# Optimization experiments

Measured on AMD Instinct MI355X. Metric: run time of the kernel, lower is better.

## Reference

```python
import jax, jax.numpy as jnp
import numpy as np

NUM_HEADS = 8
D_HEAD = 64
LN_EPS = 1e-6


def _pad_idx(lengths, max_len):
    # flat indices into a [B*max_len, ...] dense buffer for each packed token
    return np.concatenate([b * max_len + np.arange(int(l)) for b, l in enumerate(lengths)])


def _layer_norm(x, scale, bias):
    mu = jnp.mean(x, axis=-1, keepdims=True)
    var = jnp.mean(jnp.square(x - mu), axis=-1, keepdims=True)
    return (x - mu) * jax.lax.rsqrt(var + LN_EPS) * scale + bias


def setup_inputs() -> dict:
    key = jax.random.key(0)
    ks = jax.random.split(key, 12)
    d_model, d_ff, H, dh = 512, 2048, NUM_HEADS, D_HEAD
    lengths = np.array([128 * (i + 1) for i in range(8)], dtype=np.int64)  # sum = 4608
    total = int(lengths.sum())
    s = 0.02
    return {
        "x": jax.random.normal(ks[0], (total, d_model), jnp.float32),
        "mem": jax.random.normal(ks[1], (total, d_model), jnp.float32),
        "lengths_x": lengths,
        "lengths_mem": lengths.copy(),
        "Wq": jax.random.normal(ks[2], (d_model, H * dh), jnp.float32) * s,
        "Wk": jax.random.normal(ks[3], (d_model, H * dh), jnp.float32) * s,
        "Wv": jax.random.normal(ks[4], (d_model, H * dh), jnp.float32) * s,
        "Wo": jax.random.normal(ks[5], (H * dh, d_model), jnp.float32) * s,
        "ln1_scale": jnp.ones((d_model,), jnp.float32),
        "ln1_bias": jnp.zeros((d_model,), jnp.float32),
        "W1": jax.random.normal(ks[6], (d_model, d_ff), jnp.float32) * s,
        "b1": jnp.zeros((d_ff,), jnp.float32),
        "W2": jax.random.normal(ks[7], (d_ff, d_model), jnp.float32) * s,
        "b2": jnp.zeros((d_model,), jnp.float32),
        "ln2_scale": jnp.ones((d_model,), jnp.float32),
        "ln2_bias": jnp.zeros((d_model,), jnp.float32),
    }


def reference(x, mem, lengths_x, lengths_mem, Wq, Wk, Wv, Wo,
              ln1_scale, ln1_bias, W1, b1, W2, b2, ln2_scale, ln2_bias):
    lx = np.asarray(lengths_x)
    lm = np.asarray(lengths_mem)
    B = lx.shape[0]
    Lx = int(lx.max())
    Lm = int(lm.max())
    H, dh = NUM_HEADS, D_HEAD

    idx_x = _pad_idx(lx, Lx)
    idx_m = _pad_idx(lm, Lm)

    def pad(packed, idx, B, L):
        dense = jnp.zeros((B * L,) + packed.shape[1:], packed.dtype).at[idx].set(packed)
        return dense.reshape((B, L) + packed.shape[1:])

    q = pad((x @ Wq).reshape(-1, H, dh), idx_x, B, Lx)   # [B, Lx, H, dh]
    k = pad((mem @ Wk).reshape(-1, H, dh), idx_m, B, Lm)  # [B, Lm, H, dh]
    v = pad((mem @ Wv).reshape(-1, H, dh), idx_m, B, Lm)

    e = jnp.einsum('bxhd,byhd->bhxy', q, k) / np.sqrt(dh)  # [B, H, Lx, Lm]
    # validity mask: (query pos < len_x) & (key pos < len_mem)
    mask = (np.arange(Lx)[None, :, None] < lx[:, None, None]) & \
           (np.arange(Lm)[None, None, :] < lm[:, None, None])
    mask = jnp.asarray(mask)[:, None, :, :]  # [B, 1, Lx, Lm]
    e = jnp.where(mask, e, jnp.float32(-1e30))  # finite -inf surrogate; identical softmax on valid rows
    alpha = jax.nn.softmax(e, axis=-1)
    out = jnp.einsum('bhxy,byhd->bxhd', alpha, v).reshape(B, Lx, H * dh)
    out = out @ Wo                                  # [B, Lx, d_model]
    out = out.reshape(B * Lx, -1)[idx_x]            # pack back to [total_x, d_model]

    h = _layer_norm(x + out, ln1_scale, ln1_bias)
    ffn = jax.nn.relu(h @ W1 + b1) @ W2 + b2
    return _layer_norm(h + ffn, ln2_scale, ln2_bias)
```

## Files before the change

### kernel.cpp

```cpp
#include <hip/hip_runtime.h>
#include <stdint.h>

typedef short bf8v __attribute__((ext_vector_type(8)));
typedef float f4v  __attribute__((ext_vector_type(4)));
typedef short s8v  __attribute__((ext_vector_type(8)));
typedef short s4v  __attribute__((ext_vector_type(4)));
typedef int   i2v  __attribute__((ext_vector_type(2)));

__device__ __forceinline__ float bf2f(short b){
  unsigned u = ((unsigned)(unsigned short)b) << 16;
  union { unsigned u; float f; } c; c.u = u; return c.f;
}
__device__ __forceinline__ short f2bf(float f){
  union { float f; unsigned u; } c; c.f = f;
  unsigned r = (c.u + 0x7FFFu + ((c.u >> 16) & 1u)) >> 16;
  return (short)r;
}
__device__ __forceinline__ void gload16(const short* g, short* l){
  __builtin_amdgcn_global_load_lds(
      (const __attribute__((address_space(1))) void*)g,
      (__attribute__((address_space(3))) void*)l, 16, 0, 0);
}

__global__ void prep_kernel(const int* lx, const int* lm, int* meta){
  __shared__ int sjp[9], skvc[8];
  int tid = threadIdx.x;
  if (tid == 0){
    int is64 = ((lx[1] | lx[3] | lx[5] | lx[7]) == 0) ? 1 : 0;
    int ox = 0, om = 0;
    for (int b = 0; b < 8; ++b){
      int a = is64 ? lx[2*b] : lx[b];
      int c = is64 ? lm[2*b] : lm[b];
      meta[b] = a; meta[8+b] = c;
      meta[16+b] = ox; meta[25+b] = om;
      ox += a; om += c;
    }
    meta[24] = ox; meta[33] = om;
    int jp = 0;
    for (int b = 0; b < 8; ++b){
      int Lm_ = meta[8+b];
      int kvc = (Lm_ + 255) / 256; if (kvc > 4) kvc = 4; if (kvc < 1) kvc = 1;
      int clen = (((Lm_ + kvc - 1) / kvc) + 31) & ~31;
      meta[34+b] = kvc; meta[42+b] = clen;
      meta[50+b] = jp;
      sjp[b] = jp; skvc[b] = kvc;
      int qt = (meta[b] + 63) / 64;
      jp += qt * kvc * 8;
    }
    meta[58] = jp;
    sjp[8] = jp;
  }
  __syncthreads();
  int njobs = sjp[8];
  for (int j = tid; j < njobs; j += blockDim.x){
    int b = 0;
    #pragma unroll
    for (int i = 1; i < 8; ++i) if (j >= sjp[i]) b = i;
    int local = j - sjp[b];
    int kvc = skvc[b];
    int h = local & 7;
    int r = local >> 3;
    int c = r % kvc;
    int qt = r / kvc;
    meta[64+j] = b | (h << 4) | (c << 7) | (qt << 11);
  }
}

__global__ __launch_bounds__(256) void cvt2bf(const float* __restrict__ x,
                                              const float* __restrict__ mem,
                                              short* __restrict__ xb,
                                              short* __restrict__ mb,
                                              long long n){
  long long t = (long long)blockIdx.x * 256 + threadIdx.x;
  long long i = t * 8;
  const float* s; short* d;
  if (i < n){ s = x + i; d = xb + i; }
  else {
    i -= n; if (i >= n) return;
    s = mem + i; d = mb + i;
  }
  float4 f0 = *(const float4*)s;
  float4 f1 = *(const float4*)(s + 4);
  s8v o;
  o[0]=f2bf(f0.x); o[1]=f2bf(f0.y); o[2]=f2bf(f0.z); o[3]=f2bf(f0.w);
  o[4]=f2bf(f1.x); o[5]=f2bf(f1.y); o[6]=f2bf(f1.z); o[7]=f2bf(f1.w);
  *(s8v*)d = o;
}

__global__ __launch_bounds__(256) void cvt_w_t(
    const float* __restrict__ Wq, const float* __restrict__ Wk,
    const float* __restrict__ Wv, const float* __restrict__ Wo,
    const float* __restrict__ W1, const float* __restrict__ W2,
    short* __restrict__ WqT, short* __restrict__ WkT,
    short* __restrict__ WvT, short* __restrict__ WoT,
    short* __restrict__ W1T, short* __restrict__ W2T){
  __shared__ float tile[32][33];
  int bid = blockIdx.x;
  const float* W; short* WT; int K, N, t0;
  if      (bid <  256){ W=Wq; WT=WqT; K=512;  N=512;  t0=0;    }
  else if (bid <  512){ W=Wk; WT=WkT; K=512;  N=512;  t0=256;  }
  else if (bid <  768){ W=Wv; WT=WvT; K=512;  N=512;  t0=512;  }
  else if (bid < 1024){ W=Wo; WT=WoT; K=512;  N=512;  t0=768;  }
  else if (bid < 2048){ W=W1; WT=W1T; K=512;  N=2048; t0=1024; }
  else                { W=W2; WT=W2T; K=2048; N=512;  t0=2048; }
  int lt = bid - t0;
  int ntn = N / 32;
  int tk = lt / ntn, tn = lt % ntn;
  int r0 = threadIdx.x >> 5, c = threadIdx.x & 31;
  #pragma unroll
  for (int i = 0; i < 4; ++i){
    int r = r0 + i*8;
    tile[r][c] = W[(long)(tk*32 + r)*N + tn*32 + c];
  }
  __syncthreads();
  #pragma unroll
  for (int i = 0; i < 4; ++i){
    int r = r0 + i*8;
    WT[(long)(tn*32 + r)*K + tk*32 + c] = f2bf(tile[c][r]);
  }
}

__device__ __forceinline__ void stage_g64(const short* A, const short* Bt,
    long brow, long bcol, int M, int N, int K, int t,
    short* Als, short* Bls){
  int tid = threadIdx.x;
  #pragma unroll
  for (int i = 0; i < 2; ++i){
    int cc = i*256 + tid;
    int row = cc >> 3, slot = cc & 7;
    int cg = slot ^ (row & 7);
    long ar = brow + row; if (ar >= M) ar = M - 1;
    gload16(A + ar*(long)K + t + cg*8, &Als[cc*8]);
  }
  #pragma unroll
  for (int i = 0; i < 4; ++i){
    int cc = i*256 + tid;
    int row = cc >> 3, slot = cc & 7;
    int cg = slot ^ (row & 7);
    long br = bcol + row; if (br >= N) br = N - 1;
    gload16(Bt + br*(long)K + t + cg*8, &Bls[cc*8]);
  }
}

__device__ __forceinline__ void gemm_core64(const short* A, const short* Bt,
    short* __restrict__ Cb, const float* __restrict__ bias,
    int M, int N, int K, int k0, int klen,
    float scale, int relu, int colmajor,
    long brow, long bcol, short* Als, short* Bls){
  int tid = threadIdx.x;
  int lane = tid & 63, w = tid >> 6;
  int wcol = w * 32;
  int l15 = lane & 15, l4 = lane >> 4;

  f4v acc[4][2];
  #pragma unroll
  for (int m = 0; m < 4; ++m)
    #pragma unroll
    for (int n = 0; n < 2; ++n) acc[m][n] = (f4v){0.f,0.f,0.f,0.f};

  int nt = klen / 64;
  stage_g64(A, Bt, brow, bcol, M, N, K, k0, Als, Bls);
  for (int t = 0; t < nt; ++t){
    __syncthreads();
    if (t + 1 < nt)
      stage_g64(A, Bt, brow, bcol, M, N, K, k0 + (t+1)*64,
                Als + ((t+1)&1)*4096, Bls + ((t+1)&1)*8192);
    const short* Ab = Als + (t&1)*4096;
    const short* Bb = Bls + (t&1)*8192;
    bf8v a[4][2], b[2][2];
    #pragma unroll
    for (int m = 0; m < 4; ++m){
      int row = m*16 + l15;
      #pragma unroll
      for (int ks = 0; ks < 2; ++ks)
        a[m][ks] = *(const bf8v*)&Ab[row*64 + ((ks*4 + l4) ^ (row & 7))*8];
    }
    #pragma unroll
    for (int n = 0; n < 2; ++n){
      int row = wcol + n*16 + l15;
      #pragma unroll
      for (int ks = 0; ks < 2; ++ks)
        b[n][ks] = *(const bf8v*)&Bb[row*64 + ((ks*4 + l4) ^ (row & 7))*8];
    }
    #pragma unroll
    for (int m = 0; m < 4; ++m)
      #pragma unroll
      for (int n = 0; n < 2; ++n){
        acc[m][n] = __builtin_amdgcn_mfma_f32_16x16x32_bf16(a[m][0], b[n][0], acc[m][n], 0, 0, 0);
        acc[m][n] = __builtin_amdgcn_mfma_f32_16x16x32_bf16(a[m][1], b[n][1], acc[m][n], 0, 0, 0);
      }
  }

  #pragma unroll
  for (int m = 0; m < 4; ++m){
    #pragma unroll
    for (int n = 0; n < 2; ++n){
      long col = bcol + wcol + n*16 + l15;
      float bi = (bias != nullptr && col < N) ? bias[col] : 0.f;
      #pragma unroll
      for (int j = 0; j < 4; ++j){
        long row = brow + m*16 + 4*l4 + j;
        if (row < M && col < N){
          float v = acc[m][n][j] * scale + bi;
          if (relu) v = fmaxf(v, 0.f);
          Cb[colmajor ? (col*(long)M + row) : (row*(long)N + col)] = f2bf(v);
        }
      }
    }
  }
}

__global__ __launch_bounds__(256) void gemm64(
    const short* __restrict__ A, const short* __restrict__ Bt,
    short* __restrict__ C, const float* __restrict__ bias,
    int M, int N, int K, int klen, float scale, int relu, int colmajor){
  __shared__ __align__(16) short Als[2*64*64];
  __shared__ __align__(16) short Bls[2*128*64];
  int chunk = blockIdx.z;
  gemm_core64(A, Bt, C + (long)chunk * M * N, bias, M, N, K, chunk*klen, klen,
              scale, relu, colmajor,
              (long)blockIdx.y * 64, (long)blockIdx.x * 128, Als, Bls);
}

__global__ __launch_bounds__(256) void gemm_qkv(
    const short* __restrict__ xb, const short* __restrict__ mb,
    const short* __restrict__ WqT, const short* __restrict__ WkT,
    const short* __restrict__ WvT,
    short* __restrict__ Qb, short* __restrict__ Kbf, short* __restrict__ Vtb,
    int total){
  __shared__ __align__(16) short Als[2*64*64];
  __shared__ __align__(16) short Bls[2*128*64];
  int seg = blockIdx.x >> 2;
  const short* A  = (seg == 0) ? xb : mb;
  const short* Bt = (seg == 0) ? WqT : ((seg == 1) ? WkT : WvT);
  short* C        = (seg == 0) ? Qb  : ((seg == 1) ? Kbf : Vtb);
  float scale     = (seg == 0) ? 0.125f : 1.f;
  int colmajor    = (seg == 2);
  gemm_core64(A, Bt, C, nullptr, total, 512, 512, 0, 512, scale, 0, colmajor,
              (long)blockIdx.y * 64, (long)(blockIdx.x & 3) * 128, Als, Bls);
}

__global__ __launch_bounds__(256) void attn_kernel(
    const short* __restrict__ Q, const short* __restrict__ Kb,
    const short* __restrict__ Vt, short* __restrict__ Ob,
    short* __restrict__ Opart, float* __restrict__ mlpart,
    const int* __restrict__ meta, int total){
  __shared__ __align__(16) short Kls[2][32*64];
  __shared__ __align__(16) short Vls[2][64*32];
  __shared__ __align__(16) short Pls[4][16*32];
  int tid = threadIdx.x;
  int lane = tid & 63, w = tid >> 6;
  int l15 = lane & 15, l4 = lane >> 4;
  int njobs = meta[58];

  for (int j = blockIdx.x; j < njobs; j += gridDim.x){
    int word = meta[64+j];
    int b = word & 15, h = (word >> 4) & 7, c = (word >> 7) & 15, qt = word >> 11;
    int Lx = meta[b], Lm = meta[8+b];
    int ox = meta[16+b], om = meta[25+b];
    int kvc = meta[34+b], clen = meta[42+b];
    int c0 = c * clen;
    int cend = c0 + clen; if (cend > Lm) cend = Lm;
    int nt = (cend - c0 + 31) / 32;
    int qbase = qt*64 + w*16;

    __syncthreads();

    #define ATTN_STAGE(T, BUF)                                                  \
      {                                                                         \
        int kv0_ = c0 + (T)*32;                                                 \
        int kr = tid >> 3, ks_ = tid & 7;                                       \
        int cgk = ks_ ^ (kr & 7);                                               \
        int ktok = kv0_ + kr; if (ktok >= Lm) ktok = Lm - 1;                    \
        gload16(Kb + (long)(om + ktok)*512 + h*64 + cgk*8, &Kls[BUF][tid*8]);   \
        int vr = tid >> 2, vs = tid & 3;                                        \
        int cgv = vs ^ (vr & 3);                                                \
        int vkv = kv0_ + cgv*8; if (vkv + 8 > Lm) vkv = Lm - 8;                 \
        gload16(Vt + (long)(h*64 + vr)*total + om + vkv, &Vls[BUF][tid*8]);     \
      }

    ATTN_STAGE(0, 0)

    int qr = qbase + l15;
    const short* qp = Q + (long)(ox + (qr < Lx ? qr : Lx - 1))*512 + h*64 + l4*8;
    bf8v aq0 = *(const bf8v*)qp;
    bf8v aq1 = *(const bf8v*)(qp + 32);

    float mrun = -1e30f, lrun = 0.f;
    f4v o[4];
    #pragma unroll
    for (int n = 0; n < 4; ++n) o[n] = (f4v){0.f,0.f,0.f,0.f};

    for (int t = 0; t < nt; ++t){
      __syncthreads();
      if (t + 1 < nt) ATTN_STAGE(t+1, (t+1)&1)
      int buf = t & 1;
      int kv0 = c0 + t*32;

      f4v s[2];
      #pragma unroll
      for (int n = 0; n < 2; ++n){
        int krow = n*16 + l15;
        bf8v k0 = *(const bf8v*)&Kls[buf][krow*64 + ((l4    ) ^ (krow & 7))*8];
        bf8v k1 = *(const bf8v*)&Kls[buf][krow*64 + ((4 + l4) ^ (krow & 7))*8];
        f4v z = (f4v){0.f,0.f,0.f,0.f};
        z = __builtin_amdgcn_mfma_f32_16x16x32_bf16(k0, aq0, z, 0, 0, 0);
        z = __builtin_amdgcn_mfma_f32_16x16x32_bf16(k1, aq1, z, 0, 0, 0);
        s[n] = z;
      }
      if (kv0 + 32 > cend){
        #pragma unroll
        for (int n = 0; n < 2; ++n){
          int kvb = kv0 + n*16 + 4*l4;
          #pragma unroll
          for (int jj = 0; jj < 4; ++jj)
            if (kvb + jj >= cend) s[n][jj] = -1e30f;
        }
      }
      float m1 = fmaxf(fmaxf(fmaxf(s[0][0], s[0][1]), fmaxf(s[0][2], s[0][3])),
                       fmaxf(fmaxf(s[1][0], s[1][1]), fmaxf(s[1][2], s[1][3])));
      m1 = fmaxf(m1, __shfl_xor(m1, 16, 64));
      m1 = fmaxf(m1, __shfl_xor(m1, 32, 64));
      float mnew = fmaxf(mrun, m1);
      float sc = __expf(mrun - mnew);
      mrun = mnew;
      float rs = 0.f;
      #pragma unroll
      for (int n = 0; n < 2; ++n)
        #pragma unroll
        for (int jj = 0; jj < 4; ++jj){
          float p = __expf(s[n][jj] - mnew);
          s[n][jj] = p; rs += p;
        }
      rs += __shfl_xor(rs, 16, 64);
      rs += __shfl_xor(rs, 32, 64);
      lrun = lrun * sc + rs;
      #pragma unroll
      for (int n = 0; n < 4; ++n) o[n] *= sc;

      #pragma unroll
      for (int n = 0; n < 2; ++n){
        unsigned r0, r1;
        asm("v_cvt_pk_bf16_f32 %0, %1, %2" : "=v"(r0) : "v"(s[n][0]), "v"(s[n][1]));
        asm("v_cvt_pk_bf16_f32 %0, %1, %2" : "=v"(r1) : "v"(s[n][2]), "v"(s[n][3]));
        i2v pr; pr[0] = (int)r0; pr[1] = (int)r1;
        int cs = (n*4 + l4) ^ ((l15 & 3) << 1);
        *(i2v*)&Pls[w][l15*32 + cs*4] = pr;
      }
      bf8v pb = *(const bf8v*)&Pls[w][l15*32 + (((2*l4) ^ ((l15 & 3) << 1))*4)];

      #pragma unroll
      for (int n2 = 0; n2 < 4; ++n2){
        int vrow = n2*16 + l15;
        bf8v vv = *(const bf8v*)&Vls[buf][vrow*32 + ((l4 ^ (vrow & 3))*8)];
        o[n2] = __builtin_amdgcn_mfma_f32_16x16x32_bf16(vv, pb, o[n2], 0, 0, 0);
      }
    }
    #undef ATTN_STAGE

    if (qr < Lx){
      if (kvc == 1){
        float inv = 1.f / lrun;
        long obase = (long)(ox + qr)*512 + h*64;
        #pragma unroll
        for (int n2 = 0; n2 < 4; ++n2){
          s4v ov;
          #pragma unroll
          for (int jj = 0; jj < 4; ++jj) ov[jj] = f2bf(o[n2][jj] * inv);
          *(s4v*)&Ob[obase + n2*16 + l4*4] = ov;
        }
      } else {
        long slot = ((long)(ox + qr)*8 + h)*4 + c;
        #pragma unroll
        for (int n2 = 0; n2 < 4; ++n2){
          s4v ov;
          #pragma unroll
          for (int jj = 0; jj < 4; ++jj) ov[jj] = f2bf(o[n2][jj]);
          *(s4v*)&Opart[slot*64 + n2*16 + l4*4] = ov;
        }
        if (l4 == 0){
          float2 ml; ml.x = mrun; ml.y = lrun;
          *(float2*)&mlpart[slot*2] = ml;
        }
      }
    }
  }
}

__global__ __launch_bounds__(256) void attn_combine(
    const short* __restrict__ Opart, const float* __restrict__ mlpart,
    short* __restrict__ Ob, const int* __restrict__ meta, int total){
  int w = threadIdx.x >> 6, lane = threadIdx.x & 63;
  int row = blockIdx.x*4 + w;
  if (row >= total) return;
  int b = 0;
  #pragma unroll
  for (int i = 1; i < 8; ++i) if (row >= meta[16+i]) b = i;
  int kvc = meta[34+b];
  if (kvc <= 1) return;
  for (int h = 0; h < 8; ++h){
    long sbase = ((long)row*8 + h)*4;
    float m_ = -1e30f;
    for (int c = 0; c < kvc; ++c) m_ = fmaxf(m_, mlpart[(sbase+c)*2]);
    float num = 0.f, den = 0.f;
    for (int c = 0; c < kvc; ++c){
      float mc = mlpart[(sbase+c)*2];
      float lc = mlpart[(sbase+c)*2 + 1];
      float wgt = __expf(mc - m_);
      num += wgt * bf2f(Opart[(sbase+c)*64 + lane]);
      den += wgt * lc;
    }
    Ob[(long)row*512 + h*64 + lane] = f2bf(num / den);
  }
}

__global__ __launch_bounds__(256) void ln_fuse(
    const float* __restrict__ Af, const short* __restrict__ Ab,
    const short* __restrict__ PartB, int nparts, long pstride,
    const float* __restrict__ bias,
    const float* __restrict__ gamma, const float* __restrict__ beta,
    short* __restrict__ outb, float* __restrict__ outf, int rows){
  int w = threadIdx.x >> 6, lane = threadIdx.x & 63;
  long row = (long)blockIdx.x * 4 + w;
  if (row >= rows) return;
  int c0 = lane * 8;
  long base = row * 512 + c0;
  float v[8];
  if (Af){
    float4 f0 = *(const float4*)(Af + base);
    float4 f1 = *(const float4*)(Af + base + 4);
    v[0]=f0.x; v[1]=f0.y; v[2]=f0.z; v[3]=f0.w;
    v[4]=f1.x; v[5]=f1.y; v[6]=f1.z; v[7]=f1.w;
  } else {
    s8v a = *(const s8v*)(Ab + base);
    #pragma unroll
    for (int j = 0; j < 8; ++j) v[j] = bf2f(a[j]);
  }
  for (int c = 0; c < nparts; ++c){
    s8v pv = *(const s8v*)(PartB + c*pstride + base);
    #pragma unroll
    for (int j = 0; j < 8; ++j) v[j] += bf2f(pv[j]);
  }
  if (bias){
    #pragma unroll
    for (int j = 0; j < 8; ++j) v[j] += bias[c0 + j];
  }
  float sum = 0.f;
  #pragma unroll
  for (int j = 0; j < 8; ++j) sum += v[j];
  #pragma unroll
  for (int m = 1; m < 64; m <<= 1) sum += __shfl_xor(sum, m, 64);
  float mu = sum * (1.f/512.f);
  float q = 0.f;
  #pragma unroll
  for (int j = 0; j < 8; ++j){ float d = v[j] - mu; q += d*d; }
  #pragma unroll
  for (int m = 1; m < 64; m <<= 1) q += __shfl_xor(q, m, 64);
  float rs = rsqrtf(q * (1.f/512.f) + 1e-6f);
  float ov[8];
  #pragma unroll
  for (int j = 0; j < 8; ++j)
    ov[j] = (v[j] - mu) * rs * gamma[c0 + j] + beta[c0 + j];
  if (outb){
    s8v os;
    #pragma unroll
    for (int j = 0; j < 8; ++j) os[j] = f2bf(ov[j]);
    *(s8v*)(outb + base) = os;
  }
  if (outf){
    float4 f0 = {ov[0], ov[1], ov[2], ov[3]};
    float4 f1 = {ov[4], ov[5], ov[6], ov[7]};
    *(float4*)(outf + base) = f0;
    *(float4*)(outf + base + 4) = f1;
  }
}

extern "C" void kernel_launch(void* const* d_in, const int* in_sizes, int n_in,
                              void* d_out, int out_size, void* d_ws, size_t ws_size,
                              hipStream_t stream){
  (void)n_in; (void)out_size; (void)ws_size;
  const float* x   = (const float*)d_in[0];
  const float* mem = (const float*)d_in[1];
  const int*   lxr = (const int*)d_in[2];
  const int*   lmr = (const int*)d_in[3];
  const float* Wq  = (const float*)d_in[4];
  const float* Wk  = (const float*)d_in[5];
  const float* Wv  = (const float*)d_in[6];
  const float* Wo  = (const float*)d_in[7];
  const float* g1  = (const float*)d_in[8];
  const float* be1 = (const float*)d_in[9];
  const float* W1  = (const float*)d_in[10];
  const float* b1  = (const float*)d_in[11];
  const float* W2  = (const float*)d_in[12];
  const float* b2  = (const float*)d_in[13];
  const float* g2  = (const float*)d_in[14];
  const float* be2 = (const float*)d_in[15];
  float* out = (float*)d_out;

  int total = in_sizes[0] / 512;
  if (total <= 0) return;
  long long n = (long long)total * 512;

  char* p = (char*)d_ws;
  int*   meta  = (int*)p;    p += 16384;
  short* xb    = (short*)p;  p += n*2;
  short* mb    = (short*)p;  p += n*2;
  short* Qb    = (short*)p;  p += n*2;
  short* Kbf   = (short*)p;  p += n*2;
  short* Vtb   = (short*)p;  p += n*2;
  short* attnb = (short*)p;  p += n*2;
  short* hb    = (short*)p;  p += n*2;
  short* ffn1  = (short*)p;  p += (long long)total*2048*2;
  short* Opart = (short*)p;  p += (long long)total*8*4*64*2;
  float* mlprt = (float*)p;  p += (long long)total*8*4*2*4;
  short* p_wo  = (short*)p;  p += n*2*2;
  short* p_ff  = (short*)p;  p += n*4*2;
  short* WqT   = (short*)p;  p += 512*512*2;
  short* WkT   = (short*)p;  p += 512*512*2;
  short* WvT   = (short*)p;  p += 512*512*2;
  short* WoT   = (short*)p;  p += 512*512*2;
  short* W1T   = (short*)p;  p += 2048*512*2;
  short* W2T   = (short*)p;  p += 512*2048*2;

  prep_kernel<<<1, 256, 0, stream>>>(lxr, lmr, meta);

  long long th = (2*n)/8;
  cvt2bf<<<dim3((unsigned)((th + 255)/256)), dim3(256), 0, stream>>>(x, mem, xb, mb, n);
  cvt_w_t<<<dim3(3072), dim3(256), 0, stream>>>(Wq,Wk,Wv,Wo,W1,W2, WqT,WkT,WvT,WoT,W1T,W2T);

  int mt64 = (total + 63)/64;
  gemm_qkv<<<dim3(12, mt64), 256, 0, stream>>>(xb, mb, WqT, WkT, WvT, Qb, Kbf, Vtb, total);

  attn_kernel<<<dim3(2048), 256, 0, stream>>>(Qb, Kbf, Vtb, attnb,
                                              Opart, mlprt, meta, total);
  attn_combine<<<dim3((unsigned)((total + 3)/4)), 256, 0, stream>>>(
      Opart, mlprt, attnb, meta, total);

  gemm64<<<dim3(4, mt64, 2), 256, 0, stream>>>(attnb, WoT, p_wo, nullptr,
                                               total, 512, 512, 256, 1.f, 0, 0);
  ln_fuse<<<dim3((unsigned)((total + 3)/4)), 256, 0, stream>>>(
      x, nullptr, p_wo, 2, n, nullptr, g1, be1, hb, nullptr, total);

  gemm64<<<dim3(16, mt64, 1), 256, 0, stream>>>(hb, W1T, ffn1, b1,
                                                total, 2048, 512, 512, 1.f, 1, 0);
  gemm64<<<dim3(4, mt64, 4), 256, 0, stream>>>(ffn1, W2T, p_ff, nullptr,
                                               total, 512, 2048, 512, 1.f, 0, 0);
  ln_fuse<<<dim3((unsigned)((total + 3)/4)), 256, 0, stream>>>(
      nullptr, hb, p_ff, 4, n, b2, g2, be2, nullptr, out, total);
}
```

Baseline: 184.7 us.

## Merge setup kernels and stream GEMM B operand from global into registers

Fuses the metadata prep, activation bf16 conversion and weight transpose kernels into one launch, removing two kernel launches. The GEMM core is reworked to use a K-step of 32, stage only the A tile in LDS, and load B fragments straight from global memory into registers with one-step prefetch. LDS use drops to 8 KB, and launch_bounds now requests 4 blocks per SM for higher occupancy. The cost is that B loads are no longer shared through LDS, so each wave fetches its B fragments from global/L2 separately, and there are twice as many barrier iterations per K.

```diff
diff --git a/kernel.cpp b/kernel.cpp
--- a/kernel.cpp
+++ b/kernel.cpp
@@ -22,91 +22,94 @@
       (__attribute__((address_space(3))) void*)l, 16, 0, 0);
 }
 
-__global__ void prep_kernel(const int* lx, const int* lm, int* meta){
-  __shared__ int sjp[9], skvc[8];
-  int tid = threadIdx.x;
-  if (tid == 0){
-    int is64 = ((lx[1] | lx[3] | lx[5] | lx[7]) == 0) ? 1 : 0;
-    int ox = 0, om = 0;
-    for (int b = 0; b < 8; ++b){
-      int a = is64 ? lx[2*b] : lx[b];
-      int c = is64 ? lm[2*b] : lm[b];
-      meta[b] = a; meta[8+b] = c;
-      meta[16+b] = ox; meta[25+b] = om;
-      ox += a; om += c;
-    }
-    meta[24] = ox; meta[33] = om;
-    int jp = 0;
-    for (int b = 0; b < 8; ++b){
-      int Lm_ = meta[8+b];
-      int kvc = (Lm_ + 255) / 256; if (kvc > 4) kvc = 4; if (kvc < 1) kvc = 1;
-      int clen = (((Lm_ + kvc - 1) / kvc) + 31) & ~31;
-      meta[34+b] = kvc; meta[42+b] = clen;
-      meta[50+b] = jp;
-      sjp[b] = jp; skvc[b] = kvc;
-      int qt = (meta[b] + 63) / 64;
-      jp += qt * kvc * 8;
-    }
-    meta[58] = jp;
-    sjp[8] = jp;
-  }
-  __syncthreads();
-  int njobs = sjp[8];
-  for (int j = tid; j < njobs; j += blockDim.x){
-    int b = 0;
-    #pragma unroll
-    for (int i = 1; i < 8; ++i) if (j >= sjp[i]) b = i;
-    int local = j - sjp[b];
-    int kvc = skvc[b];
-    int h = local & 7;
-    int r = local >> 3;
-    int c = r % kvc;
-    int qt = r / kvc;
-    meta[64+j] = b | (h << 4) | (c << 7) | (qt << 11);
-  }
-}
-
-__global__ __launch_bounds__(256) void cvt2bf(const float* __restrict__ x,
-                                              const float* __restrict__ mem,
-                                              short* __restrict__ xb,
-                                              short* __restrict__ mb,
-                                              long long n){
-  long long t = (long long)blockIdx.x * 256 + threadIdx.x;
-  long long i = t * 8;
-  const float* s; short* d;
-  if (i < n){ s = x + i; d = xb + i; }
-  else {
-    i -= n; if (i >= n) return;
-    s = mem + i; d = mb + i;
-  }
-  float4 f0 = *(const float4*)s;
-  float4 f1 = *(const float4*)(s + 4);
-  s8v o;
-  o[0]=f2bf(f0.x); o[1]=f2bf(f0.y); o[2]=f2bf(f0.z); o[3]=f2bf(f0.w);
-  o[4]=f2bf(f1.x); o[5]=f2bf(f1.y); o[6]=f2bf(f1.z); o[7]=f2bf(f1.w);
-  *(s8v*)d = o;
-}
-
-__global__ __launch_bounds__(256) void cvt_w_t(
+__global__ __launch_bounds__(256) void setup_kernel(
+    const int* lx, const int* lm, int* meta,
+    const float* __restrict__ x, const float* __restrict__ mem,
+    short* __restrict__ xb, short* __restrict__ mb, long long n, int nblk_cvt,
     const float* __restrict__ Wq, const float* __restrict__ Wk,
     const float* __restrict__ Wv, const float* __restrict__ Wo,
     const float* __restrict__ W1, const float* __restrict__ W2,
     short* __restrict__ WqT, short* __restrict__ WkT,
     short* __restrict__ WvT, short* __restrict__ WoT,
     short* __restrict__ W1T, short* __restrict__ W2T){
+  __shared__ int sjp[9], skvc[8];
   __shared__ float tile[32][33];
+  int tid = threadIdx.x;
   int bid = blockIdx.x;
+
+  if (bid == 0){
+    if (tid == 0){
+      int is64 = ((lx[1] | lx[3] | lx[5] | lx[7]) == 0) ? 1 : 0;
+      int ox = 0, om = 0;
+      for (int b = 0; b < 8; ++b){
+        int a = is64 ? lx[2*b] : lx[b];
+        int c = is64 ? lm[2*b] : lm[b];
+        meta[b] = a; meta[8+b] = c;
+        meta[16+b] = ox; meta[25+b] = om;
+        ox += a; om += c;
+      }
+      meta[24] = ox; meta[33] = om;
+      int jp = 0;
+      for (int b = 0; b < 8; ++b){
+        int Lm_ = meta[8+b];
+        int kvc = (Lm_ + 255) / 256; if (kvc > 4) kvc = 4; if (kvc < 1) kvc = 1;
+        int clen = (((Lm_ + kvc - 1) / kvc) + 31) & ~31;
+        meta[34+b] = kvc; meta[42+b] = clen;
+        meta[50+b] = jp;
+        sjp[b] = jp; skvc[b] = kvc;
+        int qt = (meta[b] + 63) / 64;
+        jp += qt * kvc * 8;
+      }
+      meta[58] = jp;
+      sjp[8] = jp;
+    }
+    __syncthreads();
+    int njobs = sjp[8];
+    for (int j = tid; j < njobs; j += blockDim.x){
+      int b = 0;
+      #pragma unroll
+      for (int i = 1; i < 8; ++i) if (j >= sjp[i]) b = i;
+      int local = j - sjp[b];
+      int kvc = skvc[b];
+      int h = local & 7;
+      int r = local >> 3;
+      int c = r % kvc;
+      int qt = r / kvc;
+      meta[64+j] = b | (h << 4) | (c << 7) | (qt << 11);
+    }
+    return;
+  }
+
+  if (bid <= nblk_cvt){
+    long long t = (long long)(bid - 1) * 256 + tid;
+    long long i = t * 8;
+    const float* s; short* d;
+    if (i < n){ s = x + i; d = xb + i; }
+    else {
+      i -= n; if (i >= n) return;
+      s = mem + i; d = mb + i;
+    }
+    float4 f0 = *(const float4*)s;
+    float4 f1 = *(const float4*)(s + 4);
+    s8v o;
+    o[0]=f2bf(f0.x); o[1]=f2bf(f0.y); o[2]=f2bf(f0.z); o[3]=f2bf(f0.w);
+    o[4]=f2bf(f1.x); o[5]=f2bf(f1.y); o[6]=f2bf(f1.z); o[7]=f2bf(f1.w);
+    *(s8v*)d = o;
+    return;
+  }
+
+  int wbid = bid - 1 - nblk_cvt;
   const float* W; short* WT; int K, N, t0;
-  if      (bid <  256){ W=Wq; WT=WqT; K=512;  N=512;  t0=0;    }
-  else if (bid <  512){ W=Wk; WT=WkT; K=512;  N=512;  t0=256;  }
-  else if (bid <  768){ W=Wv; WT=WvT; K=512;  N=512;  t0=512;  }
-  else if (bid < 1024){ W=Wo; WT=WoT; K=512;  N=512;  t0=768;  }
-  else if (bid < 2048){ W=W1; WT=W1T; K=512;  N=2048; t0=1024; }
-  else                { W=W2; WT=W2T; K=2048; N=512;  t0=2048; }
-  int lt = bid - t0;
+  if      (wbid <  256){ W=Wq; WT=WqT; K=512;  N=512;  t0=0;    }
+  else if (wbid <  512){ W=Wk; WT=WkT; K=512;  N=512;  t0=256;  }
+  else if (wbid <  768){ W=Wv; WT=WvT; K=512;  N=512;  t0=512;  }
+  else if (wbid < 1024){ W=Wo; WT=WoT; K=512;  N=512;  t0=768;  }
+  else if (wbid < 2048){ W=W1; WT=W1T; K=512;  N=2048; t0=1024; }
+  else                 { W=W2; WT=W2T; K=2048; N=512;  t0=2048; }
+  int lt = wbid - t0;
   int ntn = N / 32;
   int tk = lt / ntn, tn = lt % ntn;
-  int r0 = threadIdx.x >> 5, c = threadIdx.x & 31;
+  int r0 = tid >> 5, c = tid & 31;
   #pragma unroll
   for (int i = 0; i < 4; ++i){
     int r = r0 + i*8;
@@ -120,33 +123,21 @@
   }
 }
 
-__device__ __forceinline__ void stage_g64(const short* A, const short* Bt,
-    long brow, long bcol, int M, int N, int K, int t,
-    short* Als, short* Bls){
+__device__ __forceinline__ void stage_a(const short* A, long brow, int M, int K,
+                                        int kofs, short* Als){
   int tid = threadIdx.x;
-  #pragma unroll
-  for (int i = 0; i < 2; ++i){
-    int cc = i*256 + tid;
-    int row = cc >> 3, slot = cc & 7;
-    int cg = slot ^ (row & 7);
-    long ar = brow + row; if (ar >= M) ar = M - 1;
-    gload16(A + ar*(long)K + t + cg*8, &Als[cc*8]);
-  }
-  #pragma unroll
-  for (int i = 0; i < 4; ++i){
-    int cc = i*256 + tid;
-    int row = cc >> 3, slot = cc & 7;
-    int cg = slot ^ (row & 7);
-    long br = bcol + row; if (br >= N) br = N - 1;
-    gload16(Bt + br*(long)K + t + cg*8, &Bls[cc*8]);
-  }
-}
-
-__device__ __forceinline__ void gemm_core64(const short* A, const short* Bt,
+  int row = tid >> 2, slot = tid & 3;
+  int cg = slot ^ ((row >> 1) & 3);
+  long ar = brow + row; if (ar >= M) ar = M - 1;
+  gload16(A + ar*(long)K + kofs + cg*8, &Als[tid*8]);
+}
+
+__device__ __forceinline__ void gemm_core(const short* __restrict__ A,
+    const short* __restrict__ Bt,
     short* __restrict__ Cb, const float* __restrict__ bias,
     int M, int N, int K, int k0, int klen,
     float scale, int relu, int colmajor,
-    long brow, long bcol, short* Als, short* Bls){
+    long brow, long bcol, short* Als){
   int tid = threadIdx.x;
   int lane = tid & 63, w = tid >> 6;
   int wcol = w * 32;
@@ -158,37 +149,34 @@
     #pragma unroll
     for (int n = 0; n < 2; ++n) acc[m][n] = (f4v){0.f,0.f,0.f,0.f};
 
-  int nt = klen / 64;
-  stage_g64(A, Bt, brow, bcol, M, N, K, k0, Als, Bls);
+  const short* bp = Bt + (bcol + wcol + l15)*(long)K + k0 + l4*8;
+  long bstep = 16*(long)K;
+
+  int nt = klen / 32;
+  stage_a(A, brow, M, K, k0, Als);
+  bf8v bc0 = *(const bf8v*)bp;
+  bf8v bc1 = *(const bf8v*)(bp + bstep);
   for (int t = 0; t < nt; ++t){
     __syncthreads();
-    if (t + 1 < nt)
-      stage_g64(A, Bt, brow, bcol, M, N, K, k0 + (t+1)*64,
-                Als + ((t+1)&1)*4096, Bls + ((t+1)&1)*8192);
-    const short* Ab = Als + (t&1)*4096;
-    const short* Bb = Bls + (t&1)*8192;
-    bf8v a[4][2], b[2][2];
+    if (t + 1 < nt) stage_a(A, brow, M, K, k0 + (t+1)*32, Als + ((t+1)&1)*2048);
+    bf8v bn0, bn1;
+    if (t + 1 < nt){
+      bn0 = *(const bf8v*)(bp + (t+1)*32);
+      bn1 = *(const bf8v*)(bp + bstep + (t+1)*32);
+    }
+    const short* Ab = Als + (t&1)*2048;
+    bf8v a[4];
     #pragma unroll
     for (int m = 0; m < 4; ++m){
       int row = m*16 + l15;
-      #pragma unroll
-      for (int ks = 0; ks < 2; ++ks)
-        a[m][ks] = *(const bf8v*)&Ab[row*64 + ((ks*4 + l4) ^ (row & 7))*8];
-    }
-    #pragma unroll
-    for (int n = 0; n < 2; ++n){
-      int row = wcol + n*16 + l15;
-      #pragma unroll
-      for (int ks = 0; ks < 2; ++ks)
-        b[n][ks] = *(const bf8v*)&Bb[row*64 + ((ks*4 + l4) ^ (row & 7))*8];
-    }
-    #pragma unroll
-    for (int m = 0; m < 4; ++m)
-      #pragma unroll
-      for (int n = 0; n < 2; ++n){
-        acc[m][n] = __builtin_amdgcn_mfma_f32_16x16x32_bf16(a[m][0], b[n][0], acc[m][n], 0, 0, 0);
-        acc[m][n] = __builtin_amdgcn_mfma_f32_16x16x32_bf16(a[m][1], b[n][1], acc[m][n], 0, 0, 0);
-      }
+      a[m] = *(const bf8v*)&Ab[row*32 + (l4 ^ ((row >> 1) & 3))*8];
+    }
+    #pragma unroll
+    for (int m = 0; m < 4; ++m){
+      acc[m][0] = __builtin_amdgcn_mfma_f32_16x16x32_bf16(a[m], bc0, acc[m][0], 0, 0, 0);
+      acc[m][1] = __builtin_amdgcn_mfma_f32_16x16x32_bf16(a[m], bc1, acc[m][1], 0, 0, 0);
+    }
+    bc0 = bn0; bc1 = bn1;
   }
 
   #pragma unroll
@@ -210,34 +198,32 @@
   }
 }
 
-__global__ __launch_bounds__(256) void gemm64(
+__global__ __launch_bounds__(256, 4) void gemm64(
     const short* __restrict__ A, const short* __restrict__ Bt,
     short* __restrict__ C, const float* __restrict__ bias,
     int M, int N, int K, int klen, float scale, int relu, int colmajor){
-  __shared__ __align__(16) short Als[2*64*64];
-  __shared__ __align__(16) short Bls[2*128*64];
+  __shared__ __align__(16) short Als[2*64*32];
   int chunk = blockIdx.z;
-  gemm_core64(A, Bt, C + (long)chunk * M * N, bias, M, N, K, chunk*klen, klen,
-              scale, relu, colmajor,
-              (long)blockIdx.y * 64, (long)blockIdx.x * 128, Als, Bls);
-}
-
-__global__ __launch_bounds__(256) void gemm_qkv(
+  gemm_core(A, Bt, C + (long)chunk * M * N, bias, M, N, K, chunk*klen, klen,
+            scale, relu, colmajor,
+            (long)blockIdx.y * 64, (long)blockIdx.x * 128, Als);
+}
+
+__global__ __launch_bounds__(256, 4) void gemm_qkv(
     const short* __restrict__ xb, const short* __restrict__ mb,
     const short* __restrict__ WqT, const short* __restrict__ WkT,
     const short* __restrict__ WvT,
     short* __restrict__ Qb, short* __restrict__ Kbf, short* __restrict__ Vtb,
     int total){
-  __shared__ __align__(16) short Als[2*64*64];
-  __shared__ __align__(16) short Bls[2*128*64];
+  __shared__ __align__(16) short Als[2*64*32];
   int seg = blockIdx.x >> 2;
   const short* A  = (seg == 0) ? xb : mb;
   const short* Bt = (seg == 0) ? WqT : ((seg == 1) ? WkT : WvT);
   short* C        = (seg == 0) ? Qb  : ((seg == 1) ? Kbf : Vtb);
   float scale     = (seg == 0) ? 0.125f : 1.f;
   int colmajor    = (seg == 2);
-  gemm_core64(A, Bt, C, nullptr, total, 512, 512, 0, 512, scale, 0, colmajor,
-              (long)blockIdx.y * 64, (long)(blockIdx.x & 3) * 128, Als, Bls);
+  gemm_core(A, Bt, C, nullptr, total, 512, 512, 0, 512, scale, 0, colmajor,
+            (long)blockIdx.y * 64, (long)(blockIdx.x & 3) * 128, Als);
 }
 
 __global__ __launch_bounds__(256) void attn_kernel(
@@ -522,11 +508,10 @@
   short* W1T   = (short*)p;  p += 2048*512*2;
   short* W2T   = (short*)p;  p += 512*2048*2;
 
-  prep_kernel<<<1, 256, 0, stream>>>(lxr, lmr, meta);
-
-  long long th = (2*n)/8;
-  cvt2bf<<<dim3((unsigned)((th + 255)/256)), dim3(256), 0, stream>>>(x, mem, xb, mb, n);
-  cvt_w_t<<<dim3(3072), dim3(256), 0, stream>>>(Wq,Wk,Wv,Wo,W1,W2, WqT,WkT,WvT,WoT,W1T,W2T);
+  int nblk_cvt = (int)(((2*n)/8 + 255) / 256);
+  setup_kernel<<<dim3((unsigned)(1 + nblk_cvt + 3072)), 256, 0, stream>>>(
+      lxr, lmr, meta, x, mem, xb, mb, n, nblk_cvt,
+      Wq, Wk, Wv, Wo, W1, W2, WqT, WkT, WvT, WoT, W1T, W2T);
 
   int mt64 = (total + 63)/64;
   gemm_qkv<<<dim3(12, mt64), 256, 0, stream>>>(xb, mb, WqT, WkT, WvT, Qb, Kbf, Vtb, total);
```

New measurement: 192.7 us. 1.04x slower.
